# Optimization experiments

Measured on AMD Instinct MI355X. Metric: run time of the kernel, lower is better.

The kernel has to match this reference:

```python
import jax, jax.numpy as jnp
import numpy as np

N = 50000      # num nodes
E = 1600000    # num edges (before self-loops)
DIN, DH, DOUT = 256, 128, 64


def _gcn_norm(edge_index, num_nodes):
    # Add self-loops, then symmetric normalization 1/sqrt(deg_i * deg_j)
    loop = jnp.arange(num_nodes, dtype=edge_index.dtype)
    src = jnp.concatenate([edge_index[0], loop])  # [E+N]
    dst = jnp.concatenate([edge_index[1], loop])  # [E+N]
    deg = jax.ops.segment_sum(jnp.ones_like(dst, dtype=jnp.float32), dst,
                              num_segments=num_nodes)
    dinv = jnp.where(deg > 0, jax.lax.rsqrt(deg), 0.0)
    norm = dinv[src] * dinv[dst]  # [E+N]
    return src, dst, norm


def _gcn_conv(x, src, dst, norm, W, b, num_nodes):
    h = x @ W                                  # [N, out] dense transform first
    msg = h[src] * norm[:, None]               # gather + scale  [E+N, out]
    out = jax.ops.segment_sum(msg, dst, num_segments=num_nodes)  # scatter-add
    return out + b


def reference(x, edge_index, W1, b1, W2, b2):
    num_nodes = x.shape[0]
    src, dst, norm = _gcn_norm(edge_index, num_nodes)
    h = _gcn_conv(x, src, dst, norm, W1, b1, num_nodes)
    h = jax.nn.relu(h)
    # dropout(p=0.5) is identity in eval mode
    out = _gcn_conv(h, src, dst, norm, W2, b2, num_nodes)
    return out


def setup_inputs() -> dict:
    key = jax.random.key(0)
    ks = jax.random.split(key, 6)
    x = jax.random.normal(ks[0], (N, DIN), dtype=jnp.float32)
    edge_index = jax.random.randint(ks[1], (2, E), 0, N, dtype=jnp.int32)
    W1 = jax.random.normal(ks[2], (DIN, DH), dtype=jnp.float32) * (1.0 / np.sqrt(DIN))
    b1 = jnp.zeros((DH,), dtype=jnp.float32)
    W2 = jax.random.normal(ks[3], (DH, DOUT), dtype=jnp.float32) * (1.0 / np.sqrt(DH))
    b2 = jnp.zeros((DOUT,), dtype=jnp.float32)
    return {"x": x, "edge_index": edge_index, "W1": W1, "b1": b1, "W2": W2, "b2": b2}
```

## Files before the change

### kernel.cpp

```cpp
#include <hip/hip_runtime.h>

#define DIN 256
#define DH  128
#define DOUT 64
#define BSH  7
#define BNODES 128
#define MAXBUK 400
#define NBLK 512

typedef unsigned int  u32;
typedef unsigned short u16;
typedef __attribute__((ext_vector_type(8))) short bf16x8;
typedef __attribute__((ext_vector_type(4))) float f32x4;

__device__ inline u16 f2bf(float f) {
  u32 u = __float_as_uint(f);
  u32 r = u + 0x7FFF + ((u >> 16) & 1);
  return (u16)(r >> 16);
}
__device__ inline float bf2f_lo(u32 packed) { return __uint_as_float(packed << 16); }
__device__ inline float bf2f_hi(u32 packed) { return __uint_as_float(packed & 0xFFFF0000u); }


__global__ __launch_bounds__(256) void hist_kernel(const int* __restrict__ dst,
    int* __restrict__ counts, int E, int nbuk) {
  __shared__ int h[MAXBUK];
  int tid = threadIdx.x, b = blockIdx.x;
  for (int i = tid; i < nbuk; i += 256) h[i] = 0;
  __syncthreads();
  int ech = (E + NBLK - 1) / NBLK;
  int e0 = b * ech, e1 = min(E, e0 + ech);
  for (int e = e0 + tid; e < e1; e += 256)
    atomicAdd(&h[dst[e] >> BSH], 1);
  __syncthreads();
  for (int i = tid; i < nbuk; i += 256) counts[(size_t)i * NBLK + b] = h[i];
}

__global__ __launch_bounds__(256) void col_scan(int* __restrict__ counts,
    int* __restrict__ colsum, int nbuk) {
  __shared__ int sm[256];
  __shared__ int carry;
  int buk = blockIdx.x, t = threadIdx.x;
  if (t == 0) carry = 0;
  __syncthreads();
  int* row = counts + (size_t)buk * NBLK;
  for (int base = 0; base < NBLK; base += 256) {
    int v = row[base + t];
    sm[t] = v;
    __syncthreads();
    for (int d = 1; d < 256; d <<= 1) {
      int a = (t >= d) ? sm[t - d] : 0;
      __syncthreads();
      sm[t] += a;
      __syncthreads();
    }
    int excl = sm[t] - v + carry;
    row[base + t] = excl;
    __syncthreads();
    if (t == 255) carry = excl + v;
    __syncthreads();
  }
  if (t == 0) colsum[buk] = carry;
}

__global__ __launch_bounds__(256) void scan_block(int* partial, int* total_out, int nb, int n) {
  __shared__ int sm[256];
  __shared__ int carry;
  int t = threadIdx.x;
  if (t == 0) carry = 0;
  __syncthreads();
  for (int base = 0; base < nb; base += 256) {
    int g = base + t;
    int v = (g < nb) ? partial[g] : 0;
    sm[t] = v;
    __syncthreads();
    for (int d = 1; d < 256; d <<= 1) {
      int add = (t >= d) ? sm[t - d] : 0;
      __syncthreads();
      sm[t] += add;
      __syncthreads();
    }
    int excl = sm[t] - v + carry;
    if (g < nb) partial[g] = excl;
    __syncthreads();
    if (t == 255) carry = excl + v;
    __syncthreads();
  }
  if (t == 0) total_out[n] = carry;
}

__global__ __launch_bounds__(256) void scatter_kernel(const int* __restrict__ src,
    const int* __restrict__ dst, const int* __restrict__ counts,
    const int* __restrict__ bb, u32* __restrict__ ebuf, int E, int nbuk) {
  __shared__ int cur[MAXBUK];
  int tid = threadIdx.x, b = blockIdx.x;
  for (int i = tid; i < nbuk; i += 256)
    cur[i] = bb[i] + counts[(size_t)i * NBLK + b];
  __syncthreads();
  int ech = (E + NBLK - 1) / NBLK;
  int e0 = b * ech, e1 = min(E, e0 + ech);
  for (int e = e0 + tid; e < e1; e += 256) {
    int d = dst[e];
    int r = atomicAdd(&cur[d >> BSH], 1);
    ebuf[r] = (u32)src[e] | ((u32)(d & (BNODES - 1)) << 16);
  }
}

__global__ __launch_bounds__(256) void bucket_node_count(const u32* __restrict__ ebuf,
    const int* __restrict__ bb, int* __restrict__ cnt, int N) {
  __shared__ int c[BNODES];
  int b = blockIdx.x, tid = threadIdx.x;
  if (tid < BNODES) c[tid] = 0;
  __syncthreads();
  int e0 = bb[b], e1 = bb[b + 1];
  for (int e = e0 + tid; e < e1; e += 256)
    atomicAdd(&c[ebuf[e] >> 16], 1);
  __syncthreads();
  int node = b * BNODES + tid;
  if (tid < BNODES && node < N) cnt[node] = c[tid];
}

__global__ __launch_bounds__(256) void reduce_chunks(const int* __restrict__ cnt,
                                                     int* __restrict__ partial, int n) {
  int t = threadIdx.x;
  int g = blockIdx.x * 256 + t;
  int v = (g < n) ? cnt[g] : 0;
  #pragma unroll
  for (int o = 32; o > 0; o >>= 1) v += __shfl_down(v, o, 64);
  __shared__ int sm[4];
  if ((t & 63) == 0) sm[t >> 6] = v;
  __syncthreads();
  if (t == 0) partial[blockIdx.x] = sm[0] + sm[1] + sm[2] + sm[3];
}

__global__ __launch_bounds__(256) void scan_chunks(const int* __restrict__ cnt,
    const int* __restrict__ chunkoff, int* __restrict__ rowptr,
    float* __restrict__ dinv, int n) {
  __shared__ int sm[256];
  int t = threadIdx.x, g = blockIdx.x * 256 + t;
  int v = (g < n) ? cnt[g] : 0;
  sm[t] = v;
  __syncthreads();
  for (int d = 1; d < 256; d <<= 1) {
    int add = (t >= d) ? sm[t - d] : 0;
    __syncthreads();
    sm[t] += add;
    __syncthreads();
  }
  if (g < n) {
    rowptr[g] = sm[t] - v + chunkoff[blockIdx.x];
    dinv[g] = rsqrtf((float)(v + 1));
  }
}

__global__ __launch_bounds__(256) void bucket_fill(const u32* __restrict__ ebuf,
    const int* __restrict__ bb, const int* __restrict__ rowptr, int* __restrict__ csr) {
  __shared__ int c[BNODES];
  int b = blockIdx.x, tid = threadIdx.x;
  if (tid < BNODES) c[tid] = 0;
  __syncthreads();
  int e0 = bb[b], e1 = bb[b + 1];
  for (int e = e0 + tid; e < e1; e += 256) {
    u32 p = ebuf[e];
    int nl = p >> 16;
    int r = atomicAdd(&c[nl], 1);
    csr[rowptr[b * BNODES + nl] + r] = (int)(p & 0xFFFFu);
  }
}


__global__ __launch_bounds__(256) void w_prep(const float* __restrict__ W1,
    const float* __restrict__ W2, u16* __restrict__ w1t, u16* __restrict__ w2t) {
  int t = blockIdx.x * 256 + threadIdx.x;
  if (t < DH * DIN) {
    int n = t >> 8, k = t & 255;
    w1t[t] = f2bf(W1[k * DH + n]);
  } else {
    int t2 = t - DH * DIN;
    int n = t2 >> 7, k = t2 & 127;
    w2t[t2] = f2bf(W2[k * DOUT + n]);
  }
}


__global__ __launch_bounds__(256) void gemm1_mfma(const float* __restrict__ x,
    const u16* __restrict__ w1t, const float* __restrict__ dinv,
    u16* __restrict__ h1, int M) {
  __shared__ u16 As[64][72];
  __shared__ u16 Bs[128][72];
  const int tid = threadIdx.x;
  const int lane = tid & 63, w = tid >> 6;
  const int row16 = lane & 15, quad = lane >> 4;
  const int rowBase = blockIdx.x * 64;
  f32x4 acc[8];
  #pragma unroll
  for (int nt = 0; nt < 8; ++nt) acc[nt] = (f32x4)(0.f);

  for (int kt = 0; kt < DIN; kt += 64) {
    {
      int r = tid >> 2, kq = tid & 3;
      int grow = rowBase + r;
      #pragma unroll
      for (int i = 0; i < 4; ++i) {
        float4 v = make_float4(0.f, 0.f, 0.f, 0.f);
        if (grow < M) v = *(const float4*)&x[(size_t)grow * DIN + kt + kq * 16 + i * 4];
        u32 lo = (u32)f2bf(v.x) | ((u32)f2bf(v.y) << 16);
        u32 hi = (u32)f2bf(v.z) | ((u32)f2bf(v.w) << 16);
        *(uint2*)&As[r][kq * 16 + i * 4] = make_uint2(lo, hi);
      }
    }
    {
      int n = tid >> 1, half = tid & 1;
      const uint4* s = (const uint4*)&w1t[n * DIN + kt + half * 32];
      uint4* d = (uint4*)&Bs[n][half * 32];
      d[0] = s[0]; d[1] = s[1]; d[2] = s[2]; d[3] = s[3];
    }
    __syncthreads();
    #pragma unroll
    for (int ks = 0; ks < 64; ks += 32) {
      bf16x8 a = *(bf16x8*)&As[w * 16 + row16][ks + quad * 8];
      #pragma unroll
      for (int nt = 0; nt < 8; ++nt) {
        bf16x8 b = *(bf16x8*)&Bs[nt * 16 + row16][ks + quad * 8];
        acc[nt] = __builtin_amdgcn_mfma_f32_16x16x32_bf16(a, b, acc[nt], 0, 0, 0);
      }
    }
    __syncthreads();
  }
  #pragma unroll
  for (int reg = 0; reg < 4; ++reg) {
    int row = rowBase + w * 16 + quad * 4 + reg;
    if (row < M) {
      float s = dinv[row];
      #pragma unroll
      for (int nt = 0; nt < 8; ++nt)
        h1[(size_t)row * DH + nt * 16 + row16] = f2bf(acc[nt][reg] * s);
    }
  }
}


__global__ __launch_bounds__(256) void gemm2_mfma(const u16* __restrict__ g1,
    const u16* __restrict__ w2t, const float* __restrict__ dinv,
    u16* __restrict__ h2, int M) {
  __shared__ u16 As[64][136];
  __shared__ u16 Bs[64][136];
  const int tid = threadIdx.x;
  const int lane = tid & 63, w = tid >> 6;
  const int row16 = lane & 15, quad = lane >> 4;
  const int rowBase = blockIdx.x * 64;
  f32x4 acc[4];
  #pragma unroll
  for (int nt = 0; nt < 4; ++nt) acc[nt] = (f32x4)(0.f);

  #pragma unroll
  for (int i = 0; i < 4; ++i) {
    int flat = i * 256 + tid;
    int r = flat >> 4, c = flat & 15;
    int grow = rowBase + r;
    uint4 v = make_uint4(0, 0, 0, 0);
    if (grow < M) v = *(const uint4*)&g1[(size_t)grow * DH + c * 8];
    *(uint4*)&As[r][c * 8] = v;
  }
  #pragma unroll
  for (int i = 0; i < 4; ++i) {
    int flat = i * 256 + tid;
    int r = flat >> 4, c = flat & 15;
    *(uint4*)&Bs[r][c * 8] = *(const uint4*)&w2t[r * DH + c * 8];
  }
  __syncthreads();
  #pragma unroll
  for (int ks = 0; ks < 128; ks += 32) {
    bf16x8 a = *(bf16x8*)&As[w * 16 + row16][ks + quad * 8];
    #pragma unroll
    for (int nt = 0; nt < 4; ++nt) {
      bf16x8 b = *(bf16x8*)&Bs[nt * 16 + row16][ks + quad * 8];
      acc[nt] = __builtin_amdgcn_mfma_f32_16x16x32_bf16(a, b, acc[nt], 0, 0, 0);
    }
  }
  #pragma unroll
  for (int reg = 0; reg < 4; ++reg) {
    int row = rowBase + w * 16 + quad * 4 + reg;
    if (row < M) {
      float s = dinv[row];
      #pragma unroll
      for (int nt = 0; nt < 4; ++nt)
        h2[(size_t)row * DOUT + nt * 16 + row16] = f2bf(acc[nt][reg] * s);
    }
  }
}


__global__ __launch_bounds__(256) void aggregate1(const u16* __restrict__ h,
    const int* __restrict__ rowptr, const int* __restrict__ csr,
    const float* __restrict__ dinv, const float* __restrict__ bias,
    u16* __restrict__ out, int n) {
  int lane = threadIdx.x & 63;
  int node = blockIdx.x * 4 + (threadIdx.x >> 6);
  if (node >= n) return;
  node = __builtin_amdgcn_readfirstlane(node);
  float di = dinv[node];
  int c0 = lane * 2;
  u32 w0 = *(const u32*)&h[(size_t)node * DH + c0];
  float ax = bf2f_lo(w0), ay = bf2f_hi(w0);
  int p = rowptr[node], pe = rowptr[node + 1];
  for (; p + 16 <= pe; p += 16) {
    int s[16];
    #pragma unroll
    for (int j = 0; j < 16; ++j) s[j] = csr[p + j];
    #pragma unroll
    for (int j = 0; j < 16; ++j) {
      u32 w = *(const u32*)&h[(size_t)s[j] * DH + c0];
      ax += bf2f_lo(w); ay += bf2f_hi(w);
    }
  }
  for (; p + 4 <= pe; p += 4) {
    int s[4];
    #pragma unroll
    for (int j = 0; j < 4; ++j) s[j] = csr[p + j];
    #pragma unroll
    for (int j = 0; j < 4; ++j) {
      u32 w = *(const u32*)&h[(size_t)s[j] * DH + c0];
      ax += bf2f_lo(w); ay += bf2f_hi(w);
    }
  }
  for (; p < pe; ++p) {
    u32 w = *(const u32*)&h[(size_t)csr[p] * DH + c0];
    ax += bf2f_lo(w); ay += bf2f_hi(w);
  }
  ax = fmaxf(fmaf(ax, di, bias[c0]), 0.f);
  ay = fmaxf(fmaf(ay, di, bias[c0 + 1]), 0.f);
  u32 pk = (u32)f2bf(ax) | ((u32)f2bf(ay) << 16);
  *(u32*)&out[(size_t)node * DH + c0] = pk;
}

__global__ __launch_bounds__(256) void aggregate2(const u16* __restrict__ h,
    const int* __restrict__ rowptr, const int* __restrict__ csr,
    const float* __restrict__ dinv, const float* __restrict__ bias,
    float* __restrict__ out, int n) {
  int lane = threadIdx.x & 63;
  int node = blockIdx.x * 4 + (threadIdx.x >> 6);
  if (node >= n) return;
  node = __builtin_amdgcn_readfirstlane(node);
  float di = dinv[node];
  float a = __uint_as_float((u32)h[(size_t)node * DOUT + lane] << 16);
  int p = rowptr[node], pe = rowptr[node + 1];
  for (; p + 16 <= pe; p += 16) {
    int s[16];
    #pragma unroll
    for (int j = 0; j < 16; ++j) s[j] = csr[p + j];
    #pragma unroll
    for (int j = 0; j < 16; ++j)
      a += __uint_as_float((u32)h[(size_t)s[j] * DOUT + lane] << 16);
  }
  for (; p + 4 <= pe; p += 4) {
    int s[4];
    #pragma unroll
    for (int j = 0; j < 4; ++j) s[j] = csr[p + j];
    #pragma unroll
    for (int j = 0; j < 4; ++j)
      a += __uint_as_float((u32)h[(size_t)s[j] * DOUT + lane] << 16);
  }
  for (; p < pe; ++p)
    a += __uint_as_float((u32)h[(size_t)csr[p] * DOUT + lane] << 16);
  out[(size_t)node * DOUT + lane] = fmaf(a, di, bias[lane]);
}


extern "C" void kernel_launch(void* const* d_in, const int* in_sizes, int n_in,
                              void* d_out, int out_size, void* d_ws, size_t ws_size,
                              hipStream_t stream) {
  const float* x  = (const float*)d_in[0];
  const int*   ei = (const int*)d_in[1];
  const float* W1 = (const float*)d_in[2];
  const float* b1 = (const float*)d_in[3];
  const float* W2 = (const float*)d_in[4];
  const float* b2 = (const float*)d_in[5];
  float* out = (float*)d_out;

  const int N = in_sizes[0] / DIN;
  const int E = in_sizes[1] / 2;
  const int* src = ei;
  const int* dst = ei + E;
  const int NB = (N + 255) / 256;
  const int nbuk = (N + BNODES - 1) / BNODES;

  char* ws = (char*)d_ws;
  size_t o = 0;
  auto alloc = [&](size_t bytes) { size_t r = o; o += (bytes + 511) & ~(size_t)511; return r; };
  size_t colsum_o  = alloc((size_t)(nbuk + 1) * 4);
  size_t counts_o  = alloc((size_t)nbuk * NBLK * 4);
  size_t rowptr_o  = alloc((size_t)(N + 1) * 4);
  size_t partial_o = alloc((size_t)NB * 4);
  size_t dinv_o    = alloc((size_t)N * 4);
  size_t cnt_o     = alloc((size_t)N * 4);
  size_t w1t_o     = alloc((size_t)DH * DIN * 2);
  size_t w2t_o     = alloc((size_t)DOUT * DH * 2);
  size_t csr_o     = alloc((size_t)E * 4);
  size_t h1_o      = alloc((size_t)N * DH * 2);
  size_t g1_o      = alloc((size_t)N * DH * 2);
  size_t h2_o      = h1_o;
  size_t ebuf_o    = g1_o;

  int*   colsum  = (int*)(ws + colsum_o);
  int*   counts  = (int*)(ws + counts_o);
  int*   rowptr  = (int*)(ws + rowptr_o);
  int*   partial = (int*)(ws + partial_o);
  float* dinv    = (float*)(ws + dinv_o);
  int*   cnt     = (int*)(ws + cnt_o);
  u16*   w1t     = (u16*)(ws + w1t_o);
  u16*   w2t     = (u16*)(ws + w2t_o);
  int*   csr     = (int*)(ws + csr_o);
  u16*   h1      = (u16*)(ws + h1_o);
  u16*   g1      = (u16*)(ws + g1_o);
  u16*   h2      = (u16*)(ws + h2_o);
  u32*   ebuf    = (u32*)(ws + ebuf_o);

  w_prep<<<(DH * DIN + DOUT * DH) / 256, 256, 0, stream>>>(W1, W2, w1t, w2t);
  hist_kernel<<<NBLK, 256, 0, stream>>>(dst, counts, E, nbuk);
  col_scan<<<nbuk, 256, 0, stream>>>(counts, colsum, nbuk);
  scan_block<<<1, 256, 0, stream>>>(colsum, colsum, nbuk, nbuk);
  scatter_kernel<<<NBLK, 256, 0, stream>>>(src, dst, counts, colsum, ebuf, E, nbuk);
  bucket_node_count<<<nbuk, 256, 0, stream>>>(ebuf, colsum, cnt, N);
  reduce_chunks<<<NB, 256, 0, stream>>>(cnt, partial, N);
  scan_block<<<1, 256, 0, stream>>>(partial, rowptr, NB, N);
  scan_chunks<<<NB, 256, 0, stream>>>(cnt, partial, rowptr, dinv, N);
  bucket_fill<<<nbuk, 256, 0, stream>>>(ebuf, colsum, rowptr, csr);

  gemm1_mfma<<<(N + 63) / 64, 256, 0, stream>>>(x, w1t, dinv, h1, N);
  aggregate1<<<(N + 3) / 4, 256, 0, stream>>>(h1, rowptr, csr, dinv, b1, g1, N);
  gemm2_mfma<<<(N + 63) / 64, 256, 0, stream>>>(g1, w2t, dinv, h2, N);
  aggregate2<<<(N + 3) / 4, 256, 0, stream>>>(h2, rowptr, csr, dinv, b2, out, N);
}
```

Before: 248.1 us.

## Partition CSR by source range and process source-range passes across nodes

Each node's neighbour list is split into four sub-rows by source-index range (16K nodes each), and the CSR stores u16 source indices. The aggregation kernels run a fixed grid of persistent waves, each handling up to seven nodes. For each source range they process every assigned node before moving on, so the gathered feature rows fall in a smaller working set that fits in cache better. dinv is now computed in bucket_node_count. The change adds a larger prefix scan (4N entries) and a separate ebuf allocation. It risks more loop overhead and load imbalance, and it depends on N ≤ 65536 and on NWAVES*KMAX covering N.

```diff
diff --git a/kernel.cpp b/kernel.cpp
--- a/kernel.cpp
+++ b/kernel.cpp
@@ -7,6 +7,10 @@
 #define BNODES 128
 #define MAXBUK 400
 #define NBLK 512
+#define NR   4
+#define RSH  14
+#define NWAVES 8192
+#define KMAX 7
 
 typedef unsigned int  u32;
 typedef unsigned short u16;
@@ -107,17 +111,27 @@
 }
 
 __global__ __launch_bounds__(256) void bucket_node_count(const u32* __restrict__ ebuf,
-    const int* __restrict__ bb, int* __restrict__ cnt, int N) {
-  __shared__ int c[BNODES];
+    const int* __restrict__ bb, int* __restrict__ cnt, float* __restrict__ dinv, int N) {
+  __shared__ int c[BNODES * NR];
   int b = blockIdx.x, tid = threadIdx.x;
-  if (tid < BNODES) c[tid] = 0;
+  for (int i = tid; i < BNODES * NR; i += 256) c[i] = 0;
   __syncthreads();
   int e0 = bb[b], e1 = bb[b + 1];
-  for (int e = e0 + tid; e < e1; e += 256)
-    atomicAdd(&c[ebuf[e] >> 16], 1);
-  __syncthreads();
+  for (int e = e0 + tid; e < e1; e += 256) {
+    u32 p = ebuf[e];
+    int nl = p >> 16, r = (int)((p & 0xFFFFu) >> RSH);
+    atomicAdd(&c[nl * NR + r], 1);
+  }
+  __syncthreads();
+  for (int i = tid; i < BNODES * NR; i += 256) {
+    int node = b * BNODES + (i >> 2);
+    if (node < N) cnt[(size_t)b * BNODES * NR + i] = c[i];
+  }
   int node = b * BNODES + tid;
-  if (tid < BNODES && node < N) cnt[node] = c[tid];
+  if (tid < BNODES && node < N) {
+    int tot = c[tid * NR] + c[tid * NR + 1] + c[tid * NR + 2] + c[tid * NR + 3];
+    dinv[node] = rsqrtf((float)(tot + 1));
+  }
 }
 
 __global__ __launch_bounds__(256) void reduce_chunks(const int* __restrict__ cnt,
@@ -134,8 +148,7 @@
 }
 
 __global__ __launch_bounds__(256) void scan_chunks(const int* __restrict__ cnt,
-    const int* __restrict__ chunkoff, int* __restrict__ rowptr,
-    float* __restrict__ dinv, int n) {
+    const int* __restrict__ chunkoff, int* __restrict__ rowptr, int n) {
   __shared__ int sm[256];
   int t = threadIdx.x, g = blockIdx.x * 256 + t;
   int v = (g < n) ? cnt[g] : 0;
@@ -147,24 +160,26 @@
     sm[t] += add;
     __syncthreads();
   }
-  if (g < n) {
-    rowptr[g] = sm[t] - v + chunkoff[blockIdx.x];
-    dinv[g] = rsqrtf((float)(v + 1));
-  }
+  if (g < n) rowptr[g] = sm[t] - v + chunkoff[blockIdx.x];
 }
 
 __global__ __launch_bounds__(256) void bucket_fill(const u32* __restrict__ ebuf,
-    const int* __restrict__ bb, const int* __restrict__ rowptr, int* __restrict__ csr) {
-  __shared__ int c[BNODES];
+    const int* __restrict__ bb, const int* __restrict__ rowptr,
+    u16* __restrict__ csr, int N) {
+  __shared__ int c[BNODES * NR];
   int b = blockIdx.x, tid = threadIdx.x;
-  if (tid < BNODES) c[tid] = 0;
+  for (int i = tid; i < BNODES * NR; i += 256) {
+    int node = b * BNODES + (i >> 2);
+    c[i] = (node < N) ? rowptr[(size_t)b * BNODES * NR + i] : 0;
+  }
   __syncthreads();
   int e0 = bb[b], e1 = bb[b + 1];
   for (int e = e0 + tid; e < e1; e += 256) {
     u32 p = ebuf[e];
     int nl = p >> 16;
-    int r = atomicAdd(&c[nl], 1);
-    csr[rowptr[b * BNODES + nl] + r] = (int)(p & 0xFFFFu);
+    u32 s = p & 0xFFFFu;
+    int pos = atomicAdd(&c[nl * NR + (int)(s >> RSH)], 1);
+    csr[pos] = (u16)s;
   }
 }
 
@@ -291,79 +306,92 @@
 }
 
 
-__global__ __launch_bounds__(256) void aggregate1(const u16* __restrict__ h,
-    const int* __restrict__ rowptr, const int* __restrict__ csr,
+__global__ __launch_bounds__(256, 8) void aggregate1p(const u16* __restrict__ h,
+    const int* __restrict__ rowptr, const u16* __restrict__ csr,
     const float* __restrict__ dinv, const float* __restrict__ bias,
     u16* __restrict__ out, int n) {
+  const u32* h32 = (const u32*)h;
   int lane = threadIdx.x & 63;
-  int node = blockIdx.x * 4 + (threadIdx.x >> 6);
-  if (node >= n) return;
-  node = __builtin_amdgcn_readfirstlane(node);
-  float di = dinv[node];
+  int gw = __builtin_amdgcn_readfirstlane(blockIdx.x * 4 + (threadIdx.x >> 6));
+  float ax[KMAX], ay[KMAX];
+  #pragma unroll
+  for (int k = 0; k < KMAX; ++k) {
+    int nd = gw + k * NWAVES;
+    if (nd < n) {
+      u32 w0 = h32[(size_t)nd * (DH / 2) + lane];
+      ax[k] = bf2f_lo(w0); ay[k] = bf2f_hi(w0);
+    } else { ax[k] = 0.f; ay[k] = 0.f; }
+  }
+  for (int r = 0; r < NR; ++r) {
+    #pragma unroll
+    for (int k = 0; k < KMAX; ++k) {
+      int nd = gw + k * NWAVES;
+      if (nd >= n) break;
+      int p = rowptr[nd * NR + r], pe = rowptr[nd * NR + r + 1];
+      for (; p + 8 <= pe; p += 8) {
+        int s[8];
+        #pragma unroll
+        for (int j = 0; j < 8; ++j) s[j] = csr[p + j];
+        #pragma unroll
+        for (int j = 0; j < 8; ++j) {
+          u32 w = h32[(size_t)s[j] * (DH / 2) + lane];
+          ax[k] += bf2f_lo(w); ay[k] += bf2f_hi(w);
+        }
+      }
+      for (; p < pe; ++p) {
+        u32 w = h32[(size_t)csr[p] * (DH / 2) + lane];
+        ax[k] += bf2f_lo(w); ay[k] += bf2f_hi(w);
+      }
+    }
+  }
   int c0 = lane * 2;
-  u32 w0 = *(const u32*)&h[(size_t)node * DH + c0];
-  float ax = bf2f_lo(w0), ay = bf2f_hi(w0);
-  int p = rowptr[node], pe = rowptr[node + 1];
-  for (; p + 16 <= pe; p += 16) {
-    int s[16];
-    #pragma unroll
-    for (int j = 0; j < 16; ++j) s[j] = csr[p + j];
-    #pragma unroll
-    for (int j = 0; j < 16; ++j) {
-      u32 w = *(const u32*)&h[(size_t)s[j] * DH + c0];
-      ax += bf2f_lo(w); ay += bf2f_hi(w);
-    }
-  }
-  for (; p + 4 <= pe; p += 4) {
-    int s[4];
-    #pragma unroll
-    for (int j = 0; j < 4; ++j) s[j] = csr[p + j];
-    #pragma unroll
-    for (int j = 0; j < 4; ++j) {
-      u32 w = *(const u32*)&h[(size_t)s[j] * DH + c0];
-      ax += bf2f_lo(w); ay += bf2f_hi(w);
-    }
-  }
-  for (; p < pe; ++p) {
-    u32 w = *(const u32*)&h[(size_t)csr[p] * DH + c0];
-    ax += bf2f_lo(w); ay += bf2f_hi(w);
-  }
-  ax = fmaxf(fmaf(ax, di, bias[c0]), 0.f);
-  ay = fmaxf(fmaf(ay, di, bias[c0 + 1]), 0.f);
-  u32 pk = (u32)f2bf(ax) | ((u32)f2bf(ay) << 16);
-  *(u32*)&out[(size_t)node * DH + c0] = pk;
-}
-
-__global__ __launch_bounds__(256) void aggregate2(const u16* __restrict__ h,
-    const int* __restrict__ rowptr, const int* __restrict__ csr,
+  #pragma unroll
+  for (int k = 0; k < KMAX; ++k) {
+    int nd = gw + k * NWAVES;
+    if (nd < n) {
+      float di = dinv[nd];
+      float fx = fmaxf(fmaf(ax[k], di, bias[c0]), 0.f);
+      float fy = fmaxf(fmaf(ay[k], di, bias[c0 + 1]), 0.f);
+      *(u32*)&out[(size_t)nd * DH + c0] = (u32)f2bf(fx) | ((u32)f2bf(fy) << 16);
+    }
+  }
+}
+
+__global__ __launch_bounds__(256, 8) void aggregate2p(const u16* __restrict__ h,
+    const int* __restrict__ rowptr, const u16* __restrict__ csr,
     const float* __restrict__ dinv, const float* __restrict__ bias,
     float* __restrict__ out, int n) {
   int lane = threadIdx.x & 63;
-  int node = blockIdx.x * 4 + (threadIdx.x >> 6);
-  if (node >= n) return;
-  node = __builtin_amdgcn_readfirstlane(node);
-  float di = dinv[node];
-  float a = __uint_as_float((u32)h[(size_t)node * DOUT + lane] << 16);
-  int p = rowptr[node], pe = rowptr[node + 1];
-  for (; p + 16 <= pe; p += 16) {
-    int s[16];
+  int gw = __builtin_amdgcn_readfirstlane(blockIdx.x * 4 + (threadIdx.x >> 6));
+  float a[KMAX];
+  #pragma unroll
+  for (int k = 0; k < KMAX; ++k) {
+    int nd = gw + k * NWAVES;
+    a[k] = (nd < n) ? __uint_as_float((u32)h[(size_t)nd * DOUT + lane] << 16) : 0.f;
+  }
+  for (int r = 0; r < NR; ++r) {
     #pragma unroll
-    for (int j = 0; j < 16; ++j) s[j] = csr[p + j];
-    #pragma unroll
-    for (int j = 0; j < 16; ++j)
-      a += __uint_as_float((u32)h[(size_t)s[j] * DOUT + lane] << 16);
-  }
-  for (; p + 4 <= pe; p += 4) {
-    int s[4];
-    #pragma unroll
-    for (int j = 0; j < 4; ++j) s[j] = csr[p + j];
-    #pragma unroll
-    for (int j = 0; j < 4; ++j)
-      a += __uint_as_float((u32)h[(size_t)s[j] * DOUT + lane] << 16);
-  }
-  for (; p < pe; ++p)
-    a += __uint_as_float((u32)h[(size_t)csr[p] * DOUT + lane] << 16);
-  out[(size_t)node * DOUT + lane] = fmaf(a, di, bias[lane]);
+    for (int k = 0; k < KMAX; ++k) {
+      int nd = gw + k * NWAVES;
+      if (nd >= n) break;
+      int p = rowptr[nd * NR + r], pe = rowptr[nd * NR + r + 1];
+      for (; p + 8 <= pe; p += 8) {
+        int s[8];
+        #pragma unroll
+        for (int j = 0; j < 8; ++j) s[j] = csr[p + j];
+        #pragma unroll
+        for (int j = 0; j < 8; ++j)
+          a[k] += __uint_as_float((u32)h[(size_t)s[j] * DOUT + lane] << 16);
+      }
+      for (; p < pe; ++p)
+        a[k] += __uint_as_float((u32)h[(size_t)csr[p] * DOUT + lane] << 16);
+    }
+  }
+  #pragma unroll
+  for (int k = 0; k < KMAX; ++k) {
+    int nd = gw + k * NWAVES;
+    if (nd < n) out[(size_t)nd * DOUT + lane] = fmaf(a[k], dinv[nd], bias[lane]);
+  }
 }
 
 
@@ -382,25 +410,26 @@
   const int E = in_sizes[1] / 2;
   const int* src = ei;
   const int* dst = ei + E;
-  const int NB = (N + 255) / 256;
   const int nbuk = (N + BNODES - 1) / BNODES;
+  const int M2 = N * NR;
+  const int NB2 = (M2 + 255) / 256;
 
   char* ws = (char*)d_ws;
   size_t o = 0;
   auto alloc = [&](size_t bytes) { size_t r = o; o += (bytes + 511) & ~(size_t)511; return r; };
   size_t colsum_o  = alloc((size_t)(nbuk + 1) * 4);
   size_t counts_o  = alloc((size_t)nbuk * NBLK * 4);
-  size_t rowptr_o  = alloc((size_t)(N + 1) * 4);
-  size_t partial_o = alloc((size_t)NB * 4);
+  size_t rowptr_o  = alloc((size_t)(M2 + 1) * 4);
+  size_t partial_o = alloc((size_t)NB2 * 4);
   size_t dinv_o    = alloc((size_t)N * 4);
-  size_t cnt_o     = alloc((size_t)N * 4);
+  size_t cnt_o     = alloc((size_t)M2 * 4);
   size_t w1t_o     = alloc((size_t)DH * DIN * 2);
   size_t w2t_o     = alloc((size_t)DOUT * DH * 2);
-  size_t csr_o     = alloc((size_t)E * 4);
+  size_t csr_o     = alloc((size_t)E * 2);
   size_t h1_o      = alloc((size_t)N * DH * 2);
   size_t g1_o      = alloc((size_t)N * DH * 2);
+  size_t ebuf_o    = alloc((size_t)E * 4);
   size_t h2_o      = h1_o;
-  size_t ebuf_o    = g1_o;
 
   int*   colsum  = (int*)(ws + colsum_o);
   int*   counts  = (int*)(ws + counts_o);
@@ -410,7 +439,7 @@
   int*   cnt     = (int*)(ws + cnt_o);
   u16*   w1t     = (u16*)(ws + w1t_o);
   u16*   w2t     = (u16*)(ws + w2t_o);
-  int*   csr     = (int*)(ws + csr_o);
+  u16*   csr     = (u16*)(ws + csr_o);
   u16*   h1      = (u16*)(ws + h1_o);
   u16*   g1      = (u16*)(ws + g1_o);
   u16*   h2      = (u16*)(ws + h2_o);
@@ -421,14 +450,14 @@
   col_scan<<<nbuk, 256, 0, stream>>>(counts, colsum, nbuk);
   scan_block<<<1, 256, 0, stream>>>(colsum, colsum, nbuk, nbuk);
   scatter_kernel<<<NBLK, 256, 0, stream>>>(src, dst, counts, colsum, ebuf, E, nbuk);
-  bucket_node_count<<<nbuk, 256, 0, stream>>>(ebuf, colsum, cnt, N);
-  reduce_chunks<<<NB, 256, 0, stream>>>(cnt, partial, N);
-  scan_block<<<1, 256, 0, stream>>>(partial, rowptr, NB, N);
-  scan_chunks<<<NB, 256, 0, stream>>>(cnt, partial, rowptr, dinv, N);
-  bucket_fill<<<nbuk, 256, 0, stream>>>(ebuf, colsum, rowptr, csr);
+  bucket_node_count<<<nbuk, 256, 0, stream>>>(ebuf, colsum, cnt, dinv, N);
+  reduce_chunks<<<NB2, 256, 0, stream>>>(cnt, partial, M2);
+  scan_block<<<1, 256, 0, stream>>>(partial, rowptr, NB2, M2);
+  scan_chunks<<<NB2, 256, 0, stream>>>(cnt, partial, rowptr, M2);
+  bucket_fill<<<nbuk, 256, 0, stream>>>(ebuf, colsum, rowptr, csr, N);
 
   gemm1_mfma<<<(N + 63) / 64, 256, 0, stream>>>(x, w1t, dinv, h1, N);
-  aggregate1<<<(N + 3) / 4, 256, 0, stream>>>(h1, rowptr, csr, dinv, b1, g1, N);
+  aggregate1p<<<NWAVES / 4, 256, 0, stream>>>(h1, rowptr, csr, dinv, b1, g1, N);
   gemm2_mfma<<<(N + 63) / 64, 256, 0, stream>>>(g1, w2t, dinv, h2, N);
-  aggregate2<<<(N + 3) / 4, 256, 0, stream>>>(h2, rowptr, csr, dinv, b2, out, N);
-}
+  aggregate2p<<<NWAVES / 4, 256, 0, stream>>>(h2, rowptr, csr, dinv, b2, out, N);
+}
```

Result: slower. 300.8 us (+21.2%).

## Collapse CSR build into fewer kernels using atomic bucket bases and u16 indices

Applied to the files above, without the earlier changes.

Merges the weight prep into the histogram launch and replaces the separate scan passes with atomic-counter allocation of bucket and node offsets, so the CSR build drops from ten launches to four. Row pointers are no longer globally ordered, so each row carries its own count array. Column indices are stored as u16 (N < 65536), halving the index bytes read by both aggregation kernels. The non-deterministic bucket placement changes memory locality of the CSR, and ebuf now gets its own workspace region.

```diff
diff --git a/kernel.cpp b/kernel.cpp
--- a/kernel.cpp
+++ b/kernel.cpp
@@ -7,6 +7,7 @@
 #define BNODES 128
 #define MAXBUK 400
 #define NBLK 512
+#define WPREP_BLOCKS ((DH * DIN + DOUT * DH) / 256)
 
 typedef unsigned int  u32;
 typedef unsigned short u16;
@@ -22,80 +23,81 @@
 __device__ inline float bf2f_hi(u32 packed) { return __uint_as_float(packed & 0xFFFF0000u); }
 
 
-__global__ __launch_bounds__(256) void hist_kernel(const int* __restrict__ dst,
-    int* __restrict__ counts, int E, int nbuk) {
-  __shared__ int h[MAXBUK];
+__global__ __launch_bounds__(256) void hist_prep(const int* __restrict__ dst,
+    int* __restrict__ counts, const float* __restrict__ W1, const float* __restrict__ W2,
+    u16* __restrict__ w1t, u16* __restrict__ w2t, int* __restrict__ gctr,
+    int E, int nbuk) {
   int tid = threadIdx.x, b = blockIdx.x;
-  for (int i = tid; i < nbuk; i += 256) h[i] = 0;
-  __syncthreads();
-  int ech = (E + NBLK - 1) / NBLK;
-  int e0 = b * ech, e1 = min(E, e0 + ech);
-  for (int e = e0 + tid; e < e1; e += 256)
-    atomicAdd(&h[dst[e] >> BSH], 1);
-  __syncthreads();
-  for (int i = tid; i < nbuk; i += 256) counts[(size_t)i * NBLK + b] = h[i];
-}
+  if (b < NBLK) {
+    __shared__ int h[MAXBUK];
+    for (int i = tid; i < nbuk; i += 256) h[i] = 0;
+    __syncthreads();
+    int ech = (E + NBLK - 1) / NBLK;
+    int e0 = b * ech, e1 = min(E, e0 + ech);
+    for (int e = e0 + tid; e < e1; e += 256)
+      atomicAdd(&h[dst[e] >> BSH], 1);
+    __syncthreads();
+    for (int i = tid; i < nbuk; i += 256) counts[(size_t)i * NBLK + b] = h[i];
+  } else {
+    if (b == NBLK && tid < 2) gctr[tid] = 0;
+    int t = (b - NBLK) * 256 + tid;
+    if (t < DH * DIN) {
+      int n = t >> 8, k = t & 255;
+      w1t[t] = f2bf(W1[k * DH + n]);
+    } else {
+      int t2 = t - DH * DIN;
+      int n = t2 >> 7, k = t2 & 127;
+      w2t[t2] = f2bf(W2[k * DOUT + n]);
+    }
+  }
+}
+
 
 __global__ __launch_bounds__(256) void col_scan(int* __restrict__ counts,
-    int* __restrict__ colsum, int nbuk) {
+    int* __restrict__ bb, int* __restrict__ colsum, int* __restrict__ gctr, int nbuk) {
   __shared__ int sm[256];
-  __shared__ int carry;
+  __shared__ int shbase;
   int buk = blockIdx.x, t = threadIdx.x;
-  if (t == 0) carry = 0;
-  __syncthreads();
   int* row = counts + (size_t)buk * NBLK;
-  for (int base = 0; base < NBLK; base += 256) {
-    int v = row[base + t];
-    sm[t] = v;
-    __syncthreads();
-    for (int d = 1; d < 256; d <<= 1) {
-      int a = (t >= d) ? sm[t - d] : 0;
-      __syncthreads();
-      sm[t] += a;
-      __syncthreads();
-    }
-    int excl = sm[t] - v + carry;
-    row[base + t] = excl;
-    __syncthreads();
-    if (t == 255) carry = excl + v;
-    __syncthreads();
-  }
-  if (t == 0) colsum[buk] = carry;
-}
-
-__global__ __launch_bounds__(256) void scan_block(int* partial, int* total_out, int nb, int n) {
-  __shared__ int sm[256];
-  __shared__ int carry;
-  int t = threadIdx.x;
-  if (t == 0) carry = 0;
-  __syncthreads();
-  for (int base = 0; base < nb; base += 256) {
-    int g = base + t;
-    int v = (g < nb) ? partial[g] : 0;
-    sm[t] = v;
-    __syncthreads();
-    for (int d = 1; d < 256; d <<= 1) {
-      int add = (t >= d) ? sm[t - d] : 0;
-      __syncthreads();
-      sm[t] += add;
-      __syncthreads();
-    }
-    int excl = sm[t] - v + carry;
-    if (g < nb) partial[g] = excl;
-    __syncthreads();
-    if (t == 255) carry = excl + v;
-    __syncthreads();
-  }
-  if (t == 0) total_out[n] = carry;
-}
+  int v0 = row[t], v1 = row[256 + t];
+  sm[t] = v0;
+  __syncthreads();
+  for (int d = 1; d < 256; d <<= 1) {
+    int a = (t >= d) ? sm[t - d] : 0;
+    __syncthreads();
+    sm[t] += a;
+    __syncthreads();
+  }
+  int excl0 = sm[t] - v0;
+  int carry = sm[255];
+  __syncthreads();
+  sm[t] = v1;
+  __syncthreads();
+  for (int d = 1; d < 256; d <<= 1) {
+    int a = (t >= d) ? sm[t - d] : 0;
+    __syncthreads();
+    sm[t] += a;
+    __syncthreads();
+  }
+  int excl1 = sm[t] - v1 + carry;
+  int total = sm[255] + carry;
+  __syncthreads();
+  if (t == 0) shbase = atomicAdd(&gctr[0], total);
+  __syncthreads();
+  int base = shbase;
+  row[t] = base + excl0;
+  row[256 + t] = base + excl1;
+  if (t == 0) { bb[buk] = base; colsum[buk] = total; }
+}
+
 
 __global__ __launch_bounds__(256) void scatter_kernel(const int* __restrict__ src,
     const int* __restrict__ dst, const int* __restrict__ counts,
-    const int* __restrict__ bb, u32* __restrict__ ebuf, int E, int nbuk) {
+    u32* __restrict__ ebuf, int E, int nbuk) {
   __shared__ int cur[MAXBUK];
   int tid = threadIdx.x, b = blockIdx.x;
   for (int i = tid; i < nbuk; i += 256)
-    cur[i] = bb[i] + counts[(size_t)i * NBLK + b];
+    cur[i] = counts[(size_t)i * NBLK + b];
   __syncthreads();
   int ech = (E + NBLK - 1) / NBLK;
   int e0 = b * ech, e1 = min(E, e0 + ech);
@@ -106,79 +108,47 @@
   }
 }
 
-__global__ __launch_bounds__(256) void bucket_node_count(const u32* __restrict__ ebuf,
-    const int* __restrict__ bb, int* __restrict__ cnt, int N) {
-  __shared__ int c[BNODES];
+
+__global__ __launch_bounds__(256) void bucket_build(const u32* __restrict__ ebuf,
+    const int* __restrict__ bb, const int* __restrict__ colsum,
+    int* __restrict__ gctr, int* __restrict__ rowptr, int* __restrict__ cnt,
+    float* __restrict__ dinv, u16* __restrict__ csr, int N) {
+  __shared__ int cn[BNODES];
+  __shared__ int sm[BNODES];
+  __shared__ int cur[BNODES];
+  __shared__ int shbase;
   int b = blockIdx.x, tid = threadIdx.x;
-  if (tid < BNODES) c[tid] = 0;
-  __syncthreads();
-  int e0 = bb[b], e1 = bb[b + 1];
+  if (tid < BNODES) cn[tid] = 0;
+  __syncthreads();
+  int e0 = bb[b], e1 = e0 + colsum[b];
   for (int e = e0 + tid; e < e1; e += 256)
-    atomicAdd(&c[ebuf[e] >> 16], 1);
-  __syncthreads();
-  int node = b * BNODES + tid;
-  if (tid < BNODES && node < N) cnt[node] = c[tid];
-}
-
-__global__ __launch_bounds__(256) void reduce_chunks(const int* __restrict__ cnt,
-                                                     int* __restrict__ partial, int n) {
-  int t = threadIdx.x;
-  int g = blockIdx.x * 256 + t;
-  int v = (g < n) ? cnt[g] : 0;
-  #pragma unroll
-  for (int o = 32; o > 0; o >>= 1) v += __shfl_down(v, o, 64);
-  __shared__ int sm[4];
-  if ((t & 63) == 0) sm[t >> 6] = v;
-  __syncthreads();
-  if (t == 0) partial[blockIdx.x] = sm[0] + sm[1] + sm[2] + sm[3];
-}
-
-__global__ __launch_bounds__(256) void scan_chunks(const int* __restrict__ cnt,
-    const int* __restrict__ chunkoff, int* __restrict__ rowptr,
-    float* __restrict__ dinv, int n) {
-  __shared__ int sm[256];
-  int t = threadIdx.x, g = blockIdx.x * 256 + t;
-  int v = (g < n) ? cnt[g] : 0;
-  sm[t] = v;
-  __syncthreads();
-  for (int d = 1; d < 256; d <<= 1) {
-    int add = (t >= d) ? sm[t - d] : 0;
-    __syncthreads();
-    sm[t] += add;
-    __syncthreads();
-  }
-  if (g < n) {
-    rowptr[g] = sm[t] - v + chunkoff[blockIdx.x];
-    dinv[g] = rsqrtf((float)(v + 1));
-  }
-}
-
-__global__ __launch_bounds__(256) void bucket_fill(const u32* __restrict__ ebuf,
-    const int* __restrict__ bb, const int* __restrict__ rowptr, int* __restrict__ csr) {
-  __shared__ int c[BNODES];
-  int b = blockIdx.x, tid = threadIdx.x;
-  if (tid < BNODES) c[tid] = 0;
-  __syncthreads();
-  int e0 = bb[b], e1 = bb[b + 1];
+    atomicAdd(&cn[ebuf[e] >> 16], 1);
+  __syncthreads();
+  if (tid == 0) shbase = atomicAdd(&gctr[1], e1 - e0);
+  if (tid < BNODES) sm[tid] = cn[tid];
+  __syncthreads();
+  for (int d = 1; d < BNODES; d <<= 1) {
+    int a = (tid < BNODES && tid >= d) ? sm[tid - d] : 0;
+    __syncthreads();
+    if (tid < BNODES) sm[tid] += a;
+    __syncthreads();
+  }
+  int base = shbase;
+  if (tid < BNODES) {
+    int excl = sm[tid] - cn[tid];
+    cur[tid] = base + excl;
+    int node = b * BNODES + tid;
+    if (node < N) {
+      rowptr[node] = base + excl;
+      cnt[node] = cn[tid];
+      dinv[node] = rsqrtf((float)(cn[tid] + 1));
+    }
+  }
+  __syncthreads();
   for (int e = e0 + tid; e < e1; e += 256) {
     u32 p = ebuf[e];
-    int nl = p >> 16;
-    int r = atomicAdd(&c[nl], 1);
-    csr[rowptr[b * BNODES + nl] + r] = (int)(p & 0xFFFFu);
-  }
-}
-
-
-__global__ __launch_bounds__(256) void w_prep(const float* __restrict__ W1,
-    const float* __restrict__ W2, u16* __restrict__ w1t, u16* __restrict__ w2t) {
-  int t = blockIdx.x * 256 + threadIdx.x;
-  if (t < DH * DIN) {
-    int n = t >> 8, k = t & 255;
-    w1t[t] = f2bf(W1[k * DH + n]);
-  } else {
-    int t2 = t - DH * DIN;
-    int n = t2 >> 7, k = t2 & 127;
-    w2t[t2] = f2bf(W2[k * DOUT + n]);
+    int pos = atomicAdd(&cur[p >> 16], 1);
+    csr[pos] = (u16)(p & 0xFFFFu);
   }
 }
 
@@ -292,9 +262,9 @@
 
 
 __global__ __launch_bounds__(256) void aggregate1(const u16* __restrict__ h,
-    const int* __restrict__ rowptr, const int* __restrict__ csr,
-    const float* __restrict__ dinv, const float* __restrict__ bias,
-    u16* __restrict__ out, int n) {
+    const int* __restrict__ rowptr, const int* __restrict__ cnt,
+    const u16* __restrict__ csr, const float* __restrict__ dinv,
+    const float* __restrict__ bias, u16* __restrict__ out, int n) {
   int lane = threadIdx.x & 63;
   int node = blockIdx.x * 4 + (threadIdx.x >> 6);
   if (node >= n) return;
@@ -303,7 +273,7 @@
   int c0 = lane * 2;
   u32 w0 = *(const u32*)&h[(size_t)node * DH + c0];
   float ax = bf2f_lo(w0), ay = bf2f_hi(w0);
-  int p = rowptr[node], pe = rowptr[node + 1];
+  int p = rowptr[node], pe = p + cnt[node];
   for (; p + 16 <= pe; p += 16) {
     int s[16];
     #pragma unroll
@@ -330,21 +300,20 @@
   }
   ax = fmaxf(fmaf(ax, di, bias[c0]), 0.f);
   ay = fmaxf(fmaf(ay, di, bias[c0 + 1]), 0.f);
-  u32 pk = (u32)f2bf(ax) | ((u32)f2bf(ay) << 16);
-  *(u32*)&out[(size_t)node * DH + c0] = pk;
+  *(u32*)&out[(size_t)node * DH + c0] = (u32)f2bf(ax) | ((u32)f2bf(ay) << 16);
 }
 
 __global__ __launch_bounds__(256) void aggregate2(const u16* __restrict__ h,
-    const int* __restrict__ rowptr, const int* __restrict__ csr,
-    const float* __restrict__ dinv, const float* __restrict__ bias,
-    float* __restrict__ out, int n) {
+    const int* __restrict__ rowptr, const int* __restrict__ cnt,
+    const u16* __restrict__ csr, const float* __restrict__ dinv,
+    const float* __restrict__ bias, float* __restrict__ out, int n) {
   int lane = threadIdx.x & 63;
   int node = blockIdx.x * 4 + (threadIdx.x >> 6);
   if (node >= n) return;
   node = __builtin_amdgcn_readfirstlane(node);
   float di = dinv[node];
   float a = __uint_as_float((u32)h[(size_t)node * DOUT + lane] << 16);
-  int p = rowptr[node], pe = rowptr[node + 1];
+  int p = rowptr[node], pe = p + cnt[node];
   for (; p + 16 <= pe; p += 16) {
     int s[16];
     #pragma unroll
@@ -382,53 +351,50 @@
   const int E = in_sizes[1] / 2;
   const int* src = ei;
   const int* dst = ei + E;
-  const int NB = (N + 255) / 256;
   const int nbuk = (N + BNODES - 1) / BNODES;
 
   char* ws = (char*)d_ws;
   size_t o = 0;
   auto alloc = [&](size_t bytes) { size_t r = o; o += (bytes + 511) & ~(size_t)511; return r; };
-  size_t colsum_o  = alloc((size_t)(nbuk + 1) * 4);
+  size_t gctr_o    = alloc(2 * 4);
+  size_t bb_o      = alloc((size_t)nbuk * 4);
+  size_t colsum_o  = alloc((size_t)nbuk * 4);
   size_t counts_o  = alloc((size_t)nbuk * NBLK * 4);
-  size_t rowptr_o  = alloc((size_t)(N + 1) * 4);
-  size_t partial_o = alloc((size_t)NB * 4);
+  size_t rowptr_o  = alloc((size_t)N * 4);
+  size_t cnt_o     = alloc((size_t)N * 4);
   size_t dinv_o    = alloc((size_t)N * 4);
-  size_t cnt_o     = alloc((size_t)N * 4);
   size_t w1t_o     = alloc((size_t)DH * DIN * 2);
   size_t w2t_o     = alloc((size_t)DOUT * DH * 2);
-  size_t csr_o     = alloc((size_t)E * 4);
+  size_t csr_o     = alloc((size_t)E * 2);
   size_t h1_o      = alloc((size_t)N * DH * 2);
   size_t g1_o      = alloc((size_t)N * DH * 2);
+  size_t ebuf_o    = alloc((size_t)E * 4);
   size_t h2_o      = h1_o;
-  size_t ebuf_o    = g1_o;
-
+
+  int*   gctr    = (int*)(ws + gctr_o);
+  int*   bb      = (int*)(ws + bb_o);
   int*   colsum  = (int*)(ws + colsum_o);
   int*   counts  = (int*)(ws + counts_o);
   int*   rowptr  = (int*)(ws + rowptr_o);
-  int*   partial = (int*)(ws + partial_o);
+  int*   cnt     = (int*)(ws + cnt_o);
   float* dinv    = (float*)(ws + dinv_o);
-  int*   cnt     = (int*)(ws + cnt_o);
   u16*   w1t     = (u16*)(ws + w1t_o);
   u16*   w2t     = (u16*)(ws + w2t_o);
-  int*   csr     = (int*)(ws + csr_o);
+  u16*   csr     = (u16*)(ws + csr_o);
   u16*   h1      = (u16*)(ws + h1_o);
   u16*   g1      = (u16*)(ws + g1_o);
   u16*   h2      = (u16*)(ws + h2_o);
   u32*   ebuf    = (u32*)(ws + ebuf_o);
 
-  w_prep<<<(DH * DIN + DOUT * DH) / 256, 256, 0, stream>>>(W1, W2, w1t, w2t);
-  hist_kernel<<<NBLK, 256, 0, stream>>>(dst, counts, E, nbuk);
-  col_scan<<<nbuk, 256, 0, stream>>>(counts, colsum, nbuk);
-  scan_block<<<1, 256, 0, stream>>>(colsum, colsum, nbuk, nbuk);
-  scatter_kernel<<<NBLK, 256, 0, stream>>>(src, dst, counts, colsum, ebuf, E, nbuk);
-  bucket_node_count<<<nbuk, 256, 0, stream>>>(ebuf, colsum, cnt, N);
-  reduce_chunks<<<NB, 256, 0, stream>>>(cnt, partial, N);
-  scan_block<<<1, 256, 0, stream>>>(partial, rowptr, NB, N);
-  scan_chunks<<<NB, 256, 0, stream>>>(cnt, partial, rowptr, dinv, N);
-  bucket_fill<<<nbuk, 256, 0, stream>>>(ebuf, colsum, rowptr, csr);
+  hist_prep<<<NBLK + WPREP_BLOCKS, 256, 0, stream>>>(dst, counts, W1, W2, w1t, w2t,
+                                                     gctr, E, nbuk);
+  col_scan<<<nbuk, 256, 0, stream>>>(counts, bb, colsum, gctr, nbuk);
+  scatter_kernel<<<NBLK, 256, 0, stream>>>(src, dst, counts, ebuf, E, nbuk);
+  bucket_build<<<nbuk, 256, 0, stream>>>(ebuf, bb, colsum, gctr, rowptr, cnt,
+                                         dinv, csr, N);
 
   gemm1_mfma<<<(N + 63) / 64, 256, 0, stream>>>(x, w1t, dinv, h1, N);
-  aggregate1<<<(N + 3) / 4, 256, 0, stream>>>(h1, rowptr, csr, dinv, b1, g1, N);
+  aggregate1<<<(N + 3) / 4, 256, 0, stream>>>(h1, rowptr, cnt, csr, dinv, b1, g1, N);
   gemm2_mfma<<<(N + 63) / 64, 256, 0, stream>>>(g1, w2t, dinv, h2, N);
-  aggregate2<<<(N + 3) / 4, 256, 0, stream>>>(h2, rowptr, csr, dinv, b2, out, N);
-}
+  aggregate2<<<(N + 3) / 4, 256, 0, stream>>>(h2, rowptr, cnt, csr, dinv, b2, out, N);
+}
```

New measurement: 251.2 us. No clear change (+1.2%).
